# Kernel optimization log

Measured on AMD Instinct MI355X. Metric: run time of the kernel, lower is better.

## Reference

```python
import jax, jax.numpy as jnp
import numpy as np

B, F, D = 1024, 256, 64  # batch, featureNumb, featureDim


def setup_inputs() -> dict:
    key = jax.random.key(0)
    k1, k2, k3, k4 = jax.random.split(key, 4)
    feature = jax.random.normal(k1, (B, F, D), dtype=jnp.float32)
    indicator = jax.random.normal(k2, (F, D), dtype=jnp.float32)
    # QKVTransformV2(n, D, D): n stacked DxD linear maps of the indicator
    W_qk = jax.random.normal(k3, (2, D, D), dtype=jnp.float32) / np.float32(np.sqrt(D))
    W_qkv = jax.random.normal(k4, (3, D, D), dtype=jnp.float32) / np.float32(np.sqrt(D))
    return {"feature": feature, "indicator": indicator, "W_qk": W_qk, "W_qkv": W_qkv}


def reference(feature, indicator, W_qk, W_qkv):
    d = indicator.shape[-1]
    scale = jnp.asarray(1.0 / np.sqrt(d), feature.dtype)

    # --- gate branch: QKTrans + DotWeight + LTE (straight-through hard threshold) ---
    trans = jnp.einsum('fd,nde->nfe', indicator, W_qk)            # [2,F,D]
    gate_logits = jnp.einsum('id,jd->ij', trans[0], trans[1]) * scale  # [F,F]
    gate = (gate_logits > 0).astype(feature.dtype)                # LTE forward: hard 0/1 gate

    # --- QKV branch, fused form of the rank-1 outer products ---
    # Original: QKV_outer[t,i,j] = qkv[t,i] (x) qkv[t,j]  (DxD rank-1)
    #           input[b,t,i,j,:] = feature[b,i] @ QKV_outer[t,i,j]
    #                            = (feature[b,i] . qkv[t,i]) * qkv[t,j]
    qkv = jnp.einsum('fd,nde->nfe', indicator, W_qkv)             # [3,F,D]
    s = jnp.einsum('bfd,nfd->nbf', feature, qkv)                  # s[t,b,i] = feature[b,i].qkv[t,i]

    # score[b,i,j] = input[b,0,i,j,:] . input[b,1,j,i,:]
    #              = s[0,b,i] * s[1,b,j] * (qkv[1,i] . qkv[0,j])
    cross = jnp.einsum('id,jd->ij', qkv[1], qkv[0])               # [F,F]
    score = s[0][:, :, None] * s[1][:, None, :] * cross[None]     # [B,F,F]
    scoreHat = score * gate[None]                                 # [B,F,F]

    # output[b,i,:] = sum_j scoreHat[b,i,j] * value[b,i,j,:]
    #               = s[2,b,i] * sum_j scoreHat[b,i,j] * qkv[2,j,:]
    out = s[2][:, :, None] * jnp.einsum('bij,jd->bid', scoreHat, qkv[2])  # [B,F,D]
    return out
```

## Files before the change

kernel.cpp:

```cpp
#include <hip/hip_runtime.h>
#include <stdint.h>

#define B 1024
#define F 256
#define D 64

typedef __attribute__((ext_vector_type(8))) short short8;
typedef __attribute__((ext_vector_type(4))) float f32x4;

__device__ __forceinline__ short f2bf(float f) {
    unsigned u = __builtin_bit_cast(unsigned, f);
    u += 0x7fff + ((u >> 16) & 1);
    return (short)(u >> 16);
}
__device__ __forceinline__ float bf2f(short s) {
    unsigned u = ((unsigned)(unsigned short)s) << 16;
    return __builtin_bit_cast(float, u);
}
__device__ __forceinline__ unsigned pk_bf16(float a, float b) {
    unsigned ua = __builtin_bit_cast(unsigned, a) + 0x8000u;
    unsigned ub = __builtin_bit_cast(unsigned, b) + 0x8000u;
    return __builtin_amdgcn_perm(ub, ua, 0x07060302u);
}


__global__ void precompute_trans(const float* __restrict__ indicator,
                                 const float* __restrict__ W_qk,
                                 const float* __restrict__ W_qkv,
                                 float* __restrict__ trans,
                                 float* __restrict__ qkv) {
    int idx = blockIdx.x * blockDim.x + threadIdx.x;
    int n   = idx / (F * D);
    int rem = idx - n * (F * D);
    int f   = rem / D;
    int e   = rem - f * D;
    const float* W = (n < 2) ? (W_qk + n * D * D) : (W_qkv + (n - 2) * D * D);
    const float* ind = indicator + f * D;
    float acc = 0.f;
#pragma unroll 8
    for (int d = 0; d < D; ++d) acc += ind[d] * W[d * D + e];
    if (n < 2) trans[n * F * D + f * D + e] = acc;
    else       qkv[(n - 2) * F * D + f * D + e] = acc;
}

__global__ __launch_bounds__(256) void compute_Mt(const float* __restrict__ trans,
                                                  const float* __restrict__ qkv,
                                                  short* __restrict__ At,
                                                  short* __restrict__ q2K) {
    int j = blockIdx.x;
    int i = threadIdx.x;
    const float4* t0 = (const float4*)(trans + i * D);
    const float4* t1 = (const float4*)(trans + F * D + j * D);
    const float4* q1 = (const float4*)(qkv + F * D + i * D);
    const float4* q0 = (const float4*)(qkv + j * D);
    float d0 = 0.f, d1 = 0.f;
#pragma unroll
    for (int k = 0; k < D / 4; ++k) {
        float4 a = t0[k], b = t1[k], c = q1[k], e = q0[k];
        d0 += a.x * b.x + a.y * b.y + a.z * b.z + a.w * b.w;
        d1 += c.x * e.x + c.y * e.y + c.z * e.z + c.w * e.w;
    }
    float v = (d0 > 0.f) ? d1 : 0.f;
    At[((j >> 5) * F + i) * 32 + (j & 31)] = f2bf(v);
    if (j < D) q2K[((i >> 5) * D + j) * 32 + (i & 31)] = f2bf(qkv[2 * F * D + i * D + j]);
}

__global__ __launch_bounds__(256, 4) void fused_main(const float* __restrict__ feature,
                                                     const float* __restrict__ qkv,
                                                     const short* __restrict__ At,
                                                     const short* __restrict__ q2K,
                                                     float* __restrict__ out) {
    int b   = blockIdx.x;
    int tid = threadIdx.x;

    __shared__ __align__(16) short s1L[F];
    __shared__ float gL[F];

    {
        int rg = tid >> 4;
        int l  = tid & 15;
#pragma unroll 4
        for (int p = 0; p < 16; ++p) {
            int f = p * 16 + rg;
            float4 fv = ((const float4*)(feature + ((size_t)(b * F + f)) * D))[l];
            float4 q0 = ((const float4*)(qkv + f * D))[l];
            float4 q1 = ((const float4*)(qkv + F * D + f * D))[l];
            float4 q2 = ((const float4*)(qkv + 2 * F * D + f * D))[l];
            float a0 = fv.x * q0.x + fv.y * q0.y + fv.z * q0.z + fv.w * q0.w;
            float a1 = fv.x * q1.x + fv.y * q1.y + fv.z * q1.z + fv.w * q1.w;
            float a2 = fv.x * q2.x + fv.y * q2.y + fv.z * q2.z + fv.w * q2.w;
#pragma unroll
            for (int m = 1; m < 16; m <<= 1) {
                a0 += __shfl_xor(a0, m, 64);
                a1 += __shfl_xor(a1, m, 64);
                a2 += __shfl_xor(a2, m, 64);
            }
            if (l == 0) {
                gL[f]  = a0 * a2;
                s1L[f] = f2bf(a1);
            }
        }
    }
    __syncthreads();

    int wave = tid >> 6;
    int lane = tid & 63;
    int l16  = lane & 15;
    int lq   = lane >> 4;
    int kq   = lq * 8;

    f32x4 acc[4][4];
#pragma unroll
    for (int mt = 0; mt < 4; ++mt)
#pragma unroll
        for (int nt = 0; nt < 4; ++nt) acc[mt][nt] = (f32x4){0.f, 0.f, 0.f, 0.f};

    for (int jt = 0; jt < F / 32; ++jt) {
        short8 sv = *(const short8*)(s1L + jt * 32 + kq);
        float sf[8];
#pragma unroll
        for (int e = 0; e < 8; ++e) sf[e] = bf2f(sv[e]);

        short8 bfr[4];
#pragma unroll
        for (int nt = 0; nt < 4; ++nt) {
            int d = nt * 16 + l16;
            short8 qv = *(const short8*)(q2K + (jt * D + d) * 32 + kq);
            int4 packed;
            packed.x = pk_bf16(bf2f(qv[0]) * sf[0], bf2f(qv[1]) * sf[1]);
            packed.y = pk_bf16(bf2f(qv[2]) * sf[2], bf2f(qv[3]) * sf[3]);
            packed.z = pk_bf16(bf2f(qv[4]) * sf[4], bf2f(qv[5]) * sf[5]);
            packed.w = pk_bf16(bf2f(qv[6]) * sf[6], bf2f(qv[7]) * sf[7]);
            bfr[nt] = __builtin_bit_cast(short8, packed);
        }
#pragma unroll
        for (int mt = 0; mt < 4; ++mt) {
            int i = wave * 64 + mt * 16 + l16;
            short8 af = *(const short8*)(At + ((size_t)jt * F + i) * 32 + kq);
#pragma unroll
            for (int nt = 0; nt < 4; ++nt)
                acc[mt][nt] = __builtin_amdgcn_mfma_f32_16x16x32_bf16(
                    af, bfr[nt], acc[mt][nt], 0, 0, 0);
        }
    }

#pragma unroll
    for (int mt = 0; mt < 4; ++mt) {
#pragma unroll
        for (int r = 0; r < 4; ++r) {
            int i = wave * 64 + mt * 16 + lq * 4 + r;
            float gg = gL[i];
            float* orow = out + ((size_t)(b * F + i)) * D;
#pragma unroll
            for (int nt = 0; nt < 4; ++nt)
                orow[nt * 16 + l16] = gg * acc[mt][nt][r];
        }
    }
}

extern "C" void kernel_launch(void* const* d_in, const int* in_sizes, int n_in,
                              void* d_out, int out_size, void* d_ws, size_t ws_size,
                              hipStream_t stream) {
    const float* feature   = (const float*)d_in[0];
    const float* indicator = (const float*)d_in[1];
    const float* W_qk      = (const float*)d_in[2];
    const float* W_qkv     = (const float*)d_in[3];
    float* out = (float*)d_out;

    float* ws    = (float*)d_ws;
    float* trans = ws;
    float* qkv   = trans + 2 * F * D;
    short* At    = (short*)(qkv + 3 * F * D);
    short* q2K   = At + F * F;

    hipLaunchKernelGGL(precompute_trans, dim3((5 * F * D) / 256), dim3(256), 0,
                       stream, indicator, W_qk, W_qkv, trans, qkv);
    hipLaunchKernelGGL(compute_Mt, dim3(F), dim3(F), 0, stream, trans, qkv, At, q2K);
    hipLaunchKernelGGL(fused_main, dim3(B), dim3(256), 0, stream,
                       feature, qkv, At, q2K, out);
}
```

Baseline: 157.1 us.

## Split fused kernel into s-projection kernel and GEMM with per-wave column tiling

Moves the per-batch s0/s1/s2 projection out of the main kernel into its own kernel that writes gate and s1 values to workspace. The GEMM kernel now gives each wave a 16-column slice of D across all 256 rows, so each wave builds only one scaled B fragment per k-step but streams all 16 A tiles. This removes the LDS staging and the block barrier, at the cost of an extra launch, a global round trip for the s values, and more A-matrix loads per wave.

```diff
diff --git a/kernel.cpp b/kernel.cpp
--- a/kernel.cpp
+++ b/kernel.cpp
@@ -65,96 +65,86 @@
     if (j < D) q2K[((i >> 5) * D + j) * 32 + (i & 31)] = f2bf(qkv[2 * F * D + i * D + j]);
 }
 
-__global__ __launch_bounds__(256, 4) void fused_main(const float* __restrict__ feature,
-                                                     const float* __restrict__ qkv,
-                                                     const short* __restrict__ At,
-                                                     const short* __restrict__ q2K,
-                                                     float* __restrict__ out) {
-    int b   = blockIdx.x;
-    int tid = threadIdx.x;
-
-    __shared__ __align__(16) short s1L[F];
-    __shared__ float gL[F];
-
-    {
-        int rg = tid >> 4;
-        int l  = tid & 15;
+__global__ __launch_bounds__(256) void compute_s(const float* __restrict__ feature,
+                                                 const float* __restrict__ qkv,
+                                                 float* __restrict__ gS,
+                                                 short* __restrict__ s1S) {
+    int b  = blockIdx.x;
+    int rg = threadIdx.x >> 4;
+    int l  = threadIdx.x & 15;
 #pragma unroll 4
-        for (int p = 0; p < 16; ++p) {
-            int f = p * 16 + rg;
-            float4 fv = ((const float4*)(feature + ((size_t)(b * F + f)) * D))[l];
-            float4 q0 = ((const float4*)(qkv + f * D))[l];
-            float4 q1 = ((const float4*)(qkv + F * D + f * D))[l];
-            float4 q2 = ((const float4*)(qkv + 2 * F * D + f * D))[l];
-            float a0 = fv.x * q0.x + fv.y * q0.y + fv.z * q0.z + fv.w * q0.w;
-            float a1 = fv.x * q1.x + fv.y * q1.y + fv.z * q1.z + fv.w * q1.w;
-            float a2 = fv.x * q2.x + fv.y * q2.y + fv.z * q2.z + fv.w * q2.w;
+    for (int p = 0; p < 16; ++p) {
+        int f = p * 16 + rg;
+        float4 fv = ((const float4*)(feature + ((size_t)(b * F + f)) * D))[l];
+        float4 q0 = ((const float4*)(qkv + f * D))[l];
+        float4 q1 = ((const float4*)(qkv + F * D + f * D))[l];
+        float4 q2 = ((const float4*)(qkv + 2 * F * D + f * D))[l];
+        float a0 = fv.x * q0.x + fv.y * q0.y + fv.z * q0.z + fv.w * q0.w;
+        float a1 = fv.x * q1.x + fv.y * q1.y + fv.z * q1.z + fv.w * q1.w;
+        float a2 = fv.x * q2.x + fv.y * q2.y + fv.z * q2.z + fv.w * q2.w;
 #pragma unroll
-            for (int m = 1; m < 16; m <<= 1) {
-                a0 += __shfl_xor(a0, m, 64);
-                a1 += __shfl_xor(a1, m, 64);
-                a2 += __shfl_xor(a2, m, 64);
-            }
-            if (l == 0) {
-                gL[f]  = a0 * a2;
-                s1L[f] = f2bf(a1);
-            }
+        for (int m = 1; m < 16; m <<= 1) {
+            a0 += __shfl_xor(a0, m, 64);
+            a1 += __shfl_xor(a1, m, 64);
+            a2 += __shfl_xor(a2, m, 64);
+        }
+        if (l == 0) {
+            gS[b * F + f]  = a0 * a2;
+            s1S[b * F + f] = f2bf(a1);
         }
     }
-    __syncthreads();
+}
 
-    int wave = tid >> 6;
+__global__ __launch_bounds__(256, 4) void gemm_out(const short* __restrict__ At,
+                                                   const short* __restrict__ q2K,
+                                                   const float* __restrict__ gS,
+                                                   const short* __restrict__ s1S,
+                                                   float* __restrict__ out) {
+    int b    = blockIdx.x;
+    int tid  = threadIdx.x;
+    int w    = tid >> 6;
     int lane = tid & 63;
     int l16  = lane & 15;
     int lq   = lane >> 4;
     int kq   = lq * 8;
 
-    f32x4 acc[4][4];
+    f32x4 acc[16];
 #pragma unroll
-    for (int mt = 0; mt < 4; ++mt)
-#pragma unroll
-        for (int nt = 0; nt < 4; ++nt) acc[mt][nt] = (f32x4){0.f, 0.f, 0.f, 0.f};
+    for (int mt = 0; mt < 16; ++mt) acc[mt] = (f32x4){0.f, 0.f, 0.f, 0.f};
+
+    const short* s1b = s1S + b * F;
 
     for (int jt = 0; jt < F / 32; ++jt) {
-        short8 sv = *(const short8*)(s1L + jt * 32 + kq);
+        short8 sv = *(const short8*)(s1b + jt * 32 + kq);
         float sf[8];
 #pragma unroll
         for (int e = 0; e < 8; ++e) sf[e] = bf2f(sv[e]);
 
-        short8 bfr[4];
+        int d = w * 16 + l16;
+        short8 qv = *(const short8*)(q2K + (jt * D + d) * 32 + kq);
+        int4 packed;
+        packed.x = pk_bf16(bf2f(qv[0]) * sf[0], bf2f(qv[1]) * sf[1]);
+        packed.y = pk_bf16(bf2f(qv[2]) * sf[2], bf2f(qv[3]) * sf[3]);
+        packed.z = pk_bf16(bf2f(qv[4]) * sf[4], bf2f(qv[5]) * sf[5]);
+        packed.w = pk_bf16(bf2f(qv[6]) * sf[6], bf2f(qv[7]) * sf[7]);
+        short8 bfr = __builtin_bit_cast(short8, packed);
+
 #pragma unroll
-        for (int nt = 0; nt < 4; ++nt) {
-            int d = nt * 16 + l16;
-            short8 qv = *(const short8*)(q2K + (jt * D + d) * 32 + kq);
-            int4 packed;
-            packed.x = pk_bf16(bf2f(qv[0]) * sf[0], bf2f(qv[1]) * sf[1]);
-            packed.y = pk_bf16(bf2f(qv[2]) * sf[2], bf2f(qv[3]) * sf[3]);
-            packed.z = pk_bf16(bf2f(qv[4]) * sf[4], bf2f(qv[5]) * sf[5]);
-            packed.w = pk_bf16(bf2f(qv[6]) * sf[6], bf2f(qv[7]) * sf[7]);
-            bfr[nt] = __builtin_bit_cast(short8, packed);
-        }
-#pragma unroll
-        for (int mt = 0; mt < 4; ++mt) {
-            int i = wave * 64 + mt * 16 + l16;
-            short8 af = *(const short8*)(At + ((size_t)jt * F + i) * 32 + kq);
-#pragma unroll
-            for (int nt = 0; nt < 4; ++nt)
-                acc[mt][nt] = __builtin_amdgcn_mfma_f32_16x16x32_bf16(
-                    af, bfr[nt], acc[mt][nt], 0, 0, 0);
+        for (int mt = 0; mt < 16; ++mt) {
+            short8 af = *(const short8*)(At + ((size_t)jt * F + mt * 16 + l16) * 32 + kq);
+            acc[mt] = __builtin_amdgcn_mfma_f32_16x16x32_bf16(af, bfr, acc[mt], 0, 0, 0);
         }
     }
 
+    const float4* g4 = (const float4*)(gS + b * F);
 #pragma unroll
-    for (int mt = 0; mt < 4; ++mt) {
-#pragma unroll
-        for (int r = 0; r < 4; ++r) {
-            int i = wave * 64 + mt * 16 + lq * 4 + r;
-            float gg = gL[i];
-            float* orow = out + ((size_t)(b * F + i)) * D;
-#pragma unroll
-            for (int nt = 0; nt < 4; ++nt)
-                orow[nt * 16 + l16] = gg * acc[mt][nt][r];
-        }
+    for (int mt = 0; mt < 16; ++mt) {
+        float4 gg = g4[mt * 4 + lq];
+        float* obase = out + ((size_t)(b * F + mt * 16 + lq * 4)) * D + w * 16 + l16;
+        obase[0 * D] = ((const float*)&gg)[0] * acc[mt][0];
+        obase[1 * D] = ((const float*)&gg)[1] * acc[mt][1];
+        obase[2 * D] = ((const float*)&gg)[2] * acc[mt][2];
+        obase[3 * D] = ((const float*)&gg)[3] * acc[mt][3];
     }
 }
 
@@ -170,12 +160,16 @@
     float* ws    = (float*)d_ws;
     float* trans = ws;
     float* qkv   = trans + 2 * F * D;
-    short* At    = (short*)(qkv + 3 * F * D);
+    float* gS    = qkv + 3 * F * D;
+    short* At    = (short*)(gS + B * F);
     short* q2K   = At + F * F;
+    short* s1S   = q2K + (F / 32) * D * 32;
 
     hipLaunchKernelGGL(precompute_trans, dim3((5 * F * D) / 256), dim3(256), 0,
                        stream, indicator, W_qk, W_qkv, trans, qkv);
     hipLaunchKernelGGL(compute_Mt, dim3(F), dim3(F), 0, stream, trans, qkv, At, q2K);
-    hipLaunchKernelGGL(fused_main, dim3(B), dim3(256), 0, stream,
-                       feature, qkv, At, q2K, out);
+    hipLaunchKernelGGL(compute_s, dim3(B), dim3(256), 0, stream,
+                       feature, qkv, gS, s1S);
+    hipLaunchKernelGGL(gemm_out, dim3(B), dim3(256), 0, stream,
+                       At, q2K, gS, s1S, out);
 }
```

Result: slower. 174.7 us (+11.2%).
